# Performance work log

Measured on AMD Instinct MI355X. Metric: run time of the kernel, lower is better.

Reference implementation:

```python
import jax, jax.numpy as jnp
import numpy as np

N = 10000
E = 160000
F_IN = 2000
HEADS = 10
C1 = 128      # layer-1 per-head out channels
C2 = 128      # layer-2 per-head out channels (latent_dim)
NEG_SLOPE = 0.2
EPS = 1e-16


def gat_conv(x, W, att_src, att_dst, bias, src, dst, heads, out_ch, concat):
    """PyG-style GATConv (eval mode, self-loops already included in src/dst).
    x: [N, F_in]; W: [F_in, heads*out_ch]; att_*: [heads, out_ch]; bias: [out_dim].
    src/dst: [E'] edge endpoints (message flows src -> dst).
    """
    n = x.shape[0]
    h = (x @ W).reshape(n, heads, out_ch)              # [N, H, C]
    a_src = jnp.einsum('nhc,hc->nh', h, att_src)       # [N, H]
    a_dst = jnp.einsum('nhc,hc->nh', h, att_dst)       # [N, H]
    e = a_src[src] + a_dst[dst]                        # [E', H]
    e = jax.nn.leaky_relu(e, NEG_SLOPE)
    # segment softmax over incoming edges of each destination node
    m = jax.ops.segment_max(e, dst, num_segments=n)    # [N, H]
    ex = jnp.exp(e - m[dst])
    s = jax.ops.segment_sum(ex, dst, num_segments=n)   # [N, H]
    alpha = ex / (s[dst] + EPS)                        # [E', H]
    msg = h[src] * alpha[:, :, None]                   # [E', H, C]
    out = jax.ops.segment_sum(msg, dst, num_segments=n)  # [N, H, C]
    out = out.reshape(n, heads * out_ch) if concat else out.mean(axis=1)
    return out + bias


def setup_inputs() -> dict:
    key = jax.random.key(0)
    ks = jax.random.split(key, 10)
    glorot = lambda k, shape: jax.random.normal(k, shape, jnp.float32) * np.sqrt(2.0 / (shape[0] + shape[-1]))
    x = jax.random.normal(ks[0], (N, F_IN), jnp.float32)
    edge_index = jax.random.randint(ks[1], (2, E), 0, N, jnp.int64)
    W1 = glorot(ks[2], (F_IN, HEADS * C1))
    att_src1 = glorot(ks[3], (HEADS, C1))
    att_dst1 = glorot(ks[4], (HEADS, C1))
    b1 = jnp.zeros((HEADS * C1,), jnp.float32)
    W2 = glorot(ks[5], (HEADS * C1, HEADS * C2))
    att_src2 = glorot(ks[6], (HEADS, C2))
    att_dst2 = glorot(ks[7], (HEADS, C2))
    b2 = jnp.zeros((C2,), jnp.float32)
    return dict(x=x, edge_index=edge_index, W1=W1, att_src1=att_src1,
                att_dst1=att_dst1, b1=b1, W2=W2, att_src2=att_src2,
                att_dst2=att_dst2, b2=b2)


def reference(x, edge_index, W1, att_src1, att_dst1, b1, W2, att_src2, att_dst2, b2):
    n = x.shape[0]
    loops = jnp.arange(n, dtype=edge_index.dtype)
    src = jnp.concatenate([edge_index[0], loops])  # add self-loops (PyG default)
    dst = jnp.concatenate([edge_index[1], loops])
    h = jax.nn.relu(gat_conv(x, W1, att_src1, att_dst1, b1, src, dst, HEADS, C1, True))
    z = jax.nn.relu(gat_conv(h, W2, att_src2, att_dst2, b2, src, dst, HEADS, C2, False))
    return z
```

## Files before the change

kernel.cpp:

```cpp
#include <hip/hip_runtime.h>

typedef unsigned short u16;
typedef __attribute__((ext_vector_type(8))) short bf16x8;
typedef __attribute__((ext_vector_type(4))) float f32x4;
typedef __attribute__((ext_vector_type(4))) unsigned u32x4;

#define NN    10000
#define EE    160000
#define ET    170000
#define FIN   2000
#define MPAD  10112
#define K1PAD 2048
#define NH    1280
#define HEADS 10
#define NT    10
#define NWG   790

__device__ __forceinline__ u16 f32_to_bf16(float f) {
    unsigned u = __float_as_uint(f);
    unsigned r = (u + 0x7fffu + ((u >> 16) & 1u)) >> 16;
    return (u16)r;
}
__device__ __forceinline__ float bf16lo(unsigned pv) { return __uint_as_float(pv << 16); }
__device__ __forceinline__ float bf16hi(unsigned pv) { return __uint_as_float(pv & 0xffff0000u); }

__device__ __forceinline__ void gload16(const u16* g, u16* l) {
    __builtin_amdgcn_global_load_lds(
        (const __attribute__((address_space(1))) void*)g,
        (__attribute__((address_space(3))) void*)l, 16, 0, 0);
}

__global__ __launch_bounds__(256) void k_prep(const float* __restrict__ x,
                                              uint2* __restrict__ A1,
                                              const float* __restrict__ W1,
                                              u16* __restrict__ B1t) {
    __shared__ float tile[32][33];
    const int bid = blockIdx.x;
    const int t = threadIdx.x;
    if (bid < 2048) {
        const int total = MPAD * (K1PAD / 4);
        for (int idx = bid * 256 + t; idx < total; idx += 2048 * 256) {
            int r = idx >> 9;
            int c = (idx & 511) << 2;
            float4 v = make_float4(0.f, 0.f, 0.f, 0.f);
            if (r < NN && c < FIN) v = *(const float4*)(x + (size_t)r * FIN + c);
            uint2 p;
            p.x = (unsigned)f32_to_bf16(v.x) | ((unsigned)f32_to_bf16(v.y) << 16);
            p.y = (unsigned)f32_to_bf16(v.z) | ((unsigned)f32_to_bf16(v.w) << 16);
            A1[idx] = p;
        }
        return;
    }
    const int tx = t & 31, ty = t >> 5;
    int b = bid - 2048;
    int k0 = (b & 63) * 32, n0 = (b >> 6) * 32;
    #pragma unroll
    for (int i = 0; i < 32; i += 8) {
        int k = k0 + ty + i;
        tile[ty + i][tx] = (k < FIN) ? W1[(size_t)k * NH + n0 + tx] : 0.f;
    }
    __syncthreads();
    #pragma unroll
    for (int i = 0; i < 32; i += 8) {
        int n = n0 + ty + i, k = k0 + tx;
        B1t[(size_t)n * K1PAD + k] = f32_to_bf16(tile[tx][ty + i]);
    }
}

__global__ __launch_bounds__(256) void k_prepW2(const float* __restrict__ W2,
                                                u16* __restrict__ B2t) {
    __shared__ float tile[32][33];
    const int t = threadIdx.x;
    const int tx = t & 31, ty = t >> 5;
    int b = blockIdx.x;
    int k0 = (b % 40) * 32, n0 = (b / 40) * 32;
    #pragma unroll
    for (int i = 0; i < 32; i += 8)
        tile[ty + i][tx] = W2[(size_t)(k0 + ty + i) * NH + n0 + tx];
    __syncthreads();
    #pragma unroll
    for (int i = 0; i < 32; i += 8) {
        int n = n0 + ty + i, k = k0 + tx;
        B2t[(size_t)n * NH + k] = f32_to_bf16(tile[tx][ty + i]);
    }
}

__global__ __launch_bounds__(512) void k_gemm(const u16* __restrict__ A,
                                              const u16* __restrict__ Bt,
                                              u16* __restrict__ Chm,
                                              const int Kpad, const int kTiles) {
    __shared__ __attribute__((aligned(16))) u16 S[32768];
    const int bid = blockIdx.x;
    const int xcd = bid & 7, idx = bid >> 3;
    const int q = NWG >> 3, r = NWG & 7;
    const int L = (xcd < r) ? (xcd * (q + 1) + idx)
                            : (r * (q + 1) + (xcd - r) * q + idx);
    const size_t m0 = (size_t)(L / NT) * 128, n0 = (size_t)(L % NT) * 128;

    const int t = threadIdx.x;
    const int lane = t & 63;
    const int wave = t >> 6;
    const int wr = wave >> 2, wc = wave & 3;

    f32x4 acc[4][2] = {};

    const int srow = t >> 3;
    const int klocal = (((t & 7) ^ ((t >> 3) & 7)) << 3);
    const u16* aRow = A + (m0 + srow) * (size_t)Kpad + klocal;
    const u16* bRow = Bt + (n0 + srow) * (size_t)Kpad + klocal;
    const size_t rStep = (size_t)64 * Kpad;

#define STAGE(kt_, bufb_) do {                                                   \
        char* db = (char*)S + (bufb_) + wave * 1024;                             \
        const u16* aP = aRow + (size_t)(kt_) * 64;                               \
        const u16* bP = bRow + (size_t)(kt_) * 64;                               \
        gload16(aP,         (u16*)(db));                                         \
        gload16(aP + rStep, (u16*)(db + 8192));                                  \
        gload16(bP,         (u16*)(db + 16384));                                 \
        gload16(bP + rStep, (u16*)(db + 24576));                                 \
    } while (0)

    STAGE(0, 0);

    const int rl = lane & 15;
    const int kchunk = lane >> 4;
    const int xorv = (rl & 7) << 4;
    const int aBase0 = (wr * 64 + rl) * 128;
    const int bBase0 = (wc * 32 + rl) * 128;
    const char* Sb = (const char*)S;

    for (int kt = 0; kt < kTiles; ++kt) {
        asm volatile("s_waitcnt vmcnt(0)" ::: "memory");
        __builtin_amdgcn_s_barrier();
        if (kt + 1 < kTiles) STAGE(kt + 1, ((kt + 1) & 1) * 32768);
        const int bufo = (kt & 1) * 32768;
        #pragma unroll
        for (int ks = 0; ks < 2; ++ks) {
            const int px = (ks * 64 + kchunk * 16) ^ xorv;
            bf16x8 af[4], bfr[2];
            #pragma unroll
            for (int mf = 0; mf < 4; ++mf)
                af[mf] = *(const bf16x8*)(Sb + bufo + aBase0 + mf * 2048 + px);
            #pragma unroll
            for (int nf = 0; nf < 2; ++nf)
                bfr[nf] = *(const bf16x8*)(Sb + bufo + 16384 + bBase0 + nf * 2048 + px);
            #pragma unroll
            for (int mf = 0; mf < 4; ++mf)
                #pragma unroll
                for (int nf = 0; nf < 2; ++nf)
                    acc[mf][nf] = __builtin_amdgcn_mfma_f32_16x16x32_bf16(
                        af[mf], bfr[nf], acc[mf][nf], 0, 0, 0);
        }
    }
#undef STAGE

    u16* Cb = Chm + (size_t)(n0 >> 7) * (MPAD << 7);
    #pragma unroll
    for (int mf = 0; mf < 4; ++mf)
        #pragma unroll
        for (int i = 0; i < 4; ++i) {
            size_t row = m0 + wr * 64 + mf * 16 + (lane >> 4) * 4 + i;
            u16* crow = Cb + row * 128 + wc * 32 + rl;
            #pragma unroll
            for (int nf = 0; nf < 2; ++nf)
                crow[nf * 16] = f32_to_bf16(acc[mf][nf][i]);
        }
}

__global__ __launch_bounds__(256) void k_attn(const u16* __restrict__ Hhm,
                                              const float* __restrict__ att_s,
                                              const float* __restrict__ att_d,
                                              float* __restrict__ a_src,
                                              float* __restrict__ a_dst) {
    const int lane = threadIdx.x & 63;
    const int n = blockIdx.x * 4 + (threadIdx.x >> 6);
    if (n >= NN) return;
    const unsigned* Hd = (const unsigned*)Hhm;
    #pragma unroll
    for (int h = 0; h < HEADS; ++h) {
        unsigned pv = Hd[((size_t)h * MPAD + n) * 64 + lane];
        float v0 = bf16lo(pv), v1 = bf16hi(pv);
        int c = h * 128 + lane * 2;
        float s = v0 * att_s[c] + v1 * att_s[c + 1];
        float d = v0 * att_d[c] + v1 * att_d[c + 1];
        #pragma unroll
        for (int o = 32; o; o >>= 1) { s += __shfl_xor(s, o); d += __shfl_xor(d, o); }
        if (lane == 0) { a_src[h * NN + n] = s; a_dst[h * NN + n] = d; }
    }
}

__global__ void k_count(const int* __restrict__ ei, int* __restrict__ deg) {
    int e = blockIdx.x * blockDim.x + threadIdx.x;
    if (e >= ET) return;
    int d = (e < EE) ? ei[EE + e] : (e - EE);
    atomicAdd(&deg[d], 1);
}

__global__ __launch_bounds__(1024) void k_scan(const int* __restrict__ deg,
                                               int* __restrict__ off,
                                               int* __restrict__ cursor) {
    __shared__ int wt[16];
    const int t = threadIdx.x, lane = t & 63, w = t >> 6;
    const int lo = t * 10;
    const int hi = (lo + 10 < NN) ? lo + 10 : NN;
    int s = 0;
    for (int i = lo; i < hi; ++i) s += deg[i];
    int x = s;
    #pragma unroll
    for (int o = 1; o < 64; o <<= 1) { int y = __shfl_up(x, o); if (lane >= o) x += y; }
    if (lane == 63) wt[w] = x;
    __syncthreads();
    int wp = 0;
    for (int k = 0; k < w; ++k) wp += wt[k];
    int run = wp + x - s;
    for (int i = lo; i < hi; ++i) { off[i] = run; cursor[i] = run; run += deg[i]; }
    if (t == 1023) off[NN] = wp + x;
}

__global__ void k_scatter(const int* __restrict__ ei, int* __restrict__ cursor,
                          int* __restrict__ csr_src) {
    int e = blockIdx.x * blockDim.x + threadIdx.x;
    if (e >= ET) return;
    int s = (e < EE) ? ei[e] : (e - EE);
    int d = (e < EE) ? ei[EE + e] : (e - EE);
    int pos = atomicAdd(&cursor[d], 1);
    csr_src[pos] = s;
}

template <int LAYER>
__global__ __launch_bounds__(256) void k_agg(const u16* __restrict__ Hhm,
                                             const float* __restrict__ a_src,
                                             const float* __restrict__ a_dst,
                                             const int* __restrict__ off,
                                             const int* __restrict__ csr,
                                             const float* __restrict__ bias,
                                             unsigned* __restrict__ outp) {
    const int bid = blockIdx.x;
    if (LAYER == 1 && bid >= 6256) {
        int idx = (bid - 6256) * 256 + threadIdx.x;
        if (idx < 112 * 640) outp[(size_t)NN * 640 + idx] = 0u;
        return;
    }
    const int xcd = bid & 7, slot = bid >> 3;
    const int wv = threadIdx.x >> 6, lane = threadIdx.x & 63;
    const int u = slot * 4 + wv;
    if (u >= 3125) return;
    int h, qd;
    if (u < 2500) { h = xcd; qd = u; }
    else {
        int qg = xcd * 625 + (u - 2500);
        h = 8 + (qg >= 2500);
        qd = (qg >= 2500) ? qg - 2500 : qg;
    }
    const int g = lane >> 4, l = lane & 15;
    const int n = qd * 4 + g;
    const int beg = off[n], end = off[n + 1];
    const u16* Hh = Hhm + (size_t)h * (MPAD * 128);
    const float* asl = a_src + (size_t)h * NN;
    const float ad = a_dst[(size_t)h * NN + n];

    float acc[8] = {};
    float den = 0.f;
    int i = beg;
    for (; i + 3 < end; i += 4) {
        const int s0 = csr[i], s1 = csr[i + 1], s2 = csr[i + 2], s3 = csr[i + 3];
        const float a0 = asl[s0], a1 = asl[s1], a2 = asl[s2], a3 = asl[s3];
        const u32x4 v0 = *(const u32x4*)(Hh + (size_t)s0 * 128 + l * 8);
        const u32x4 v1 = *(const u32x4*)(Hh + (size_t)s1 * 128 + l * 8);
        const u32x4 v2 = *(const u32x4*)(Hh + (size_t)s2 * 128 + l * 8);
        const u32x4 v3 = *(const u32x4*)(Hh + (size_t)s3 * 128 + l * 8);
        float e0 = a0 + ad; e0 = (e0 >= 0.f) ? e0 : 0.2f * e0;
        float e1 = a1 + ad; e1 = (e1 >= 0.f) ? e1 : 0.2f * e1;
        float e2 = a2 + ad; e2 = (e2 >= 0.f) ? e2 : 0.2f * e2;
        float e3 = a3 + ad; e3 = (e3 >= 0.f) ? e3 : 0.2f * e3;
        const float w0 = __expf(e0), w1 = __expf(e1);
        const float w2 = __expf(e2), w3 = __expf(e3);
        den += (w0 + w1) + (w2 + w3);
        #pragma unroll
        for (int j = 0; j < 4; ++j) {
            acc[2 * j]     = fmaf(bf16lo(v0[j]), w0, acc[2 * j]);
            acc[2 * j + 1] = fmaf(bf16hi(v0[j]), w0, acc[2 * j + 1]);
            acc[2 * j]     = fmaf(bf16lo(v1[j]), w1, acc[2 * j]);
            acc[2 * j + 1] = fmaf(bf16hi(v1[j]), w1, acc[2 * j + 1]);
            acc[2 * j]     = fmaf(bf16lo(v2[j]), w2, acc[2 * j]);
            acc[2 * j + 1] = fmaf(bf16hi(v2[j]), w2, acc[2 * j + 1]);
            acc[2 * j]     = fmaf(bf16lo(v3[j]), w3, acc[2 * j]);
            acc[2 * j + 1] = fmaf(bf16hi(v3[j]), w3, acc[2 * j + 1]);
        }
    }
    for (; i < end; ++i) {
        const int s0 = csr[i];
        float e0 = asl[s0] + ad; e0 = (e0 >= 0.f) ? e0 : 0.2f * e0;
        const float w0 = __expf(e0);
        const u32x4 v0 = *(const u32x4*)(Hh + (size_t)s0 * 128 + l * 8);
        den += w0;
        #pragma unroll
        for (int j = 0; j < 4; ++j) {
            acc[2 * j]     = fmaf(bf16lo(v0[j]), w0, acc[2 * j]);
            acc[2 * j + 1] = fmaf(bf16hi(v0[j]), w0, acc[2 * j + 1]);
        }
    }
    const float si = 1.f / (den + 1e-16f);

    u32x4 pk;
    if (LAYER == 1) {
        const int c = h * 128 + l * 8;
        #pragma unroll
        for (int j = 0; j < 4; ++j) {
            float v0 = fmaxf(fmaf(acc[2 * j],     si, bias[c + 2 * j]),     0.f);
            float v1 = fmaxf(fmaf(acc[2 * j + 1], si, bias[c + 2 * j + 1]), 0.f);
            pk[j] = (unsigned)f32_to_bf16(v0) | ((unsigned)f32_to_bf16(v1) << 16);
        }
        *(u32x4*)(outp + (size_t)n * 640 + h * 64 + l * 4) = pk;
    } else {
        #pragma unroll
        for (int j = 0; j < 4; ++j) {
            pk[j] = (unsigned)f32_to_bf16(acc[2 * j] * si)
                  | ((unsigned)f32_to_bf16(acc[2 * j + 1] * si) << 16);
        }
        *(u32x4*)(outp + (size_t)h * (MPAD * 64) + (size_t)n * 64 + l * 4) = pk;
    }
}

__global__ __launch_bounds__(256) void k_final(const unsigned* __restrict__ Z,
                                               const float* __restrict__ b2,
                                               float* __restrict__ out) {
    int t = blockIdx.x * 256 + threadIdx.x;
    if (t >= NN * 64) return;
    int n = t >> 6, d = t & 63;
    float s0 = 0.f, s1 = 0.f;
    #pragma unroll
    for (int h = 0; h < HEADS; ++h) {
        unsigned pv = Z[(size_t)h * (MPAD * 64) + (size_t)n * 64 + d];
        s0 += bf16lo(pv);
        s1 += bf16hi(pv);
    }
    float2 z;
    z.x = fmaxf(fmaf(s0, 0.1f, b2[2 * d]),     0.f);
    z.y = fmaxf(fmaf(s1, 0.1f, b2[2 * d + 1]), 0.f);
    *(float2*)(out + (size_t)n * 128 + 2 * d) = z;
}

extern "C" void kernel_launch(void* const* d_in, const int* in_sizes, int n_in,
                              void* d_out, int out_size, void* d_ws, size_t ws_size,
                              hipStream_t stream) {
    const float* x   = (const float*)d_in[0];
    const int*   ei  = (const int*)  d_in[1];
    const float* W1  = (const float*)d_in[2];
    const float* as1 = (const float*)d_in[3];
    const float* ad1 = (const float*)d_in[4];
    const float* b1  = (const float*)d_in[5];
    const float* W2  = (const float*)d_in[6];
    const float* as2 = (const float*)d_in[7];
    const float* ad2 = (const float*)d_in[8];
    const float* b2  = (const float*)d_in[9];

    char* ws = (char*)d_ws;
    const size_t A1_OFF  = 0;
    const size_t A2_OFF  = 0;
    const size_t B2T_OFF = (size_t)MPAD * NH * 2;
    const size_t H_OFF   = (size_t)MPAD * K1PAD * 2;
    const size_t B1T_OFF = H_OFF + (size_t)MPAD * NH * 2;
    size_t o = B1T_OFF + (size_t)NH * K1PAD * 2;
    const size_t AS_OFF  = o; o += 400128;
    const size_t AD_OFF  = o; o += 400128;
    const size_t DEG_OFF = o; o += 40064;
    const size_t OFF_OFF = o; o += 40064;
    const size_t CUR_OFF = o; o += 40064;
    const size_t CSR_OFF = o; o += 680064;
    if (ws_size < o) return;

    u16*      A1   = (u16*)(ws + A1_OFF);
    unsigned* A2   = (unsigned*)(ws + A2_OFF);
    u16*      B2t  = (u16*)(ws + B2T_OFF);
    u16*      H    = (u16*)(ws + H_OFF);
    u16*      B1t  = (u16*)(ws + B1T_OFF);
    float*    aS   = (float*)(ws + AS_OFF);
    float*    aD   = (float*)(ws + AD_OFF);
    int*      deg  = (int*)(ws + DEG_OFF);
    int*      offp = (int*)(ws + OFF_OFF);
    int*      cur  = (int*)(ws + CUR_OFF);
    int*      csr  = (int*)(ws + CSR_OFF);

    hipMemsetAsync(deg, 0, NN * sizeof(int), stream);
    k_count<<<(ET + 255) / 256, 256, 0, stream>>>(ei, deg);
    k_scan<<<1, 1024, 0, stream>>>(deg, offp, cur);
    k_scatter<<<(ET + 255) / 256, 256, 0, stream>>>(ei, cur, csr);

    k_prep<<<4608, 256, 0, stream>>>(x, (uint2*)A1, W1, B1t);

    k_gemm<<<NWG, 512, 0, stream>>>(A1, B1t, H, K1PAD, K1PAD / 64);
    k_prepW2<<<1600, 256, 0, stream>>>(W2, B2t);
    k_attn<<<2500, 256, 0, stream>>>(H, as1, ad1, aS, aD);
    k_agg<1><<<6536, 256, 0, stream>>>(H, aS, aD, offp, csr, b1, A2);

    k_gemm<<<NWG, 512, 0, stream>>>((u16*)A2, B2t, H, NH, NH / 64);
    k_attn<<<2500, 256, 0, stream>>>(H, as2, ad2, aS, aD);
    k_agg<2><<<6256, 256, 0, stream>>>(H, aS, aD, offp, csr, b2, A2);
    k_final<<<(NN * 64 + 255) / 256, 256, 0, stream>>>(A2, b2, (float*)d_out);
}
```

Before: 272.2 us.

## Make each GEMM workgroup compute two adjacent N tiles sequentially

Each GEMM workgroup now handles two consecutive 128-column output tiles. It runs one continuous double-buffered K loop over both tiles and writes the first tile's results midway, so the grid halves from 790 to 395 workgroups. This is meant to cut the wave-quantization tail on 256 CUs and keep the pipeline primed across tile boundaries. The cost is fewer concurrent workgroups (395 over 256 CUs is still uneven) and longer serial work per workgroup, with no reuse of A between the two tiles.

```diff
diff --git a/kernel.cpp b/kernel.cpp
--- a/kernel.cpp
+++ b/kernel.cpp
@@ -14,7 +14,7 @@
 #define NH    1280
 #define HEADS 10
 #define NT    10
-#define NWG   790
+#define NWG2  395
 
 __device__ __forceinline__ u16 f32_to_bf16(float f) {
     unsigned u = __float_as_uint(f);
@@ -92,10 +92,12 @@
     __shared__ __attribute__((aligned(16))) u16 S[32768];
     const int bid = blockIdx.x;
     const int xcd = bid & 7, idx = bid >> 3;
-    const int q = NWG >> 3, r = NWG & 7;
-    const int L = (xcd < r) ? (xcd * (q + 1) + idx)
-                            : (r * (q + 1) + (xcd - r) * q + idx);
-    const size_t m0 = (size_t)(L / NT) * 128, n0 = (size_t)(L % NT) * 128;
+    const int q = NWG2 >> 3, rr = NWG2 & 7;
+    const int P = (xcd < rr) ? (xcd * (q + 1) + idx)
+                             : (rr * (q + 1) + (xcd - rr) * q + idx);
+    const int L0 = 2 * P;
+    const size_t m0 = (size_t)(L0 / NT) * 128;
+    const int n0a = (L0 % NT) * 128;
 
     const int t = threadIdx.x;
     const int lane = t & 63;
@@ -107,17 +109,34 @@
     const int srow = t >> 3;
     const int klocal = (((t & 7) ^ ((t >> 3) & 7)) << 3);
     const u16* aRow = A + (m0 + srow) * (size_t)Kpad + klocal;
-    const u16* bRow = Bt + (n0 + srow) * (size_t)Kpad + klocal;
+    const u16* bRow = Bt + (size_t)(n0a + srow) * Kpad + klocal;
     const size_t rStep = (size_t)64 * Kpad;
-
-#define STAGE(kt_, bufb_) do {                                                   \
+    const size_t bTile = (size_t)128 * Kpad;
+
+#define STAGE(j_, bufb_) do {                                                    \
         char* db = (char*)S + (bufb_) + wave * 1024;                             \
-        const u16* aP = aRow + (size_t)(kt_) * 64;                               \
-        const u16* bP = bRow + (size_t)(kt_) * 64;                               \
+        const int jj_ = (j_) < kTiles ? (j_) : (j_) - kTiles;                    \
+        const u16* bR_ = (j_) < kTiles ? bRow : bRow + bTile;                    \
+        const u16* aP = aRow + (size_t)jj_ * 64;                                 \
+        const u16* bP = bR_ + (size_t)jj_ * 64;                                  \
         gload16(aP,         (u16*)(db));                                         \
         gload16(aP + rStep, (u16*)(db + 8192));                                  \
         gload16(bP,         (u16*)(db + 16384));                                 \
         gload16(bP + rStep, (u16*)(db + 24576));                                 \
+    } while (0)
+
+#define EPILOG(ncol_) do {                                                       \
+        u16* Cb_ = Chm + (size_t)((ncol_) >> 7) * (MPAD << 7);                   \
+        _Pragma("unroll")                                                        \
+        for (int mf_ = 0; mf_ < 4; ++mf_)                                        \
+            _Pragma("unroll")                                                    \
+            for (int i_ = 0; i_ < 4; ++i_) {                                     \
+                size_t row_ = m0 + wr * 64 + mf_ * 16 + (lane >> 4) * 4 + i_;    \
+                u16* crow_ = Cb_ + row_ * 128 + wc * 32 + (lane & 15);           \
+                _Pragma("unroll")                                                \
+                for (int nf_ = 0; nf_ < 2; ++nf_)                                \
+                    crow_[nf_ * 16] = f32_to_bf16(acc[mf_][nf_][i_]);            \
+            }                                                                    \
     } while (0)
 
     STAGE(0, 0);
@@ -128,11 +147,12 @@
     const int aBase0 = (wr * 64 + rl) * 128;
     const int bBase0 = (wc * 32 + rl) * 128;
     const char* Sb = (const char*)S;
-
-    for (int kt = 0; kt < kTiles; ++kt) {
+    const int kTotal = 2 * kTiles;
+
+    for (int kt = 0; kt < kTotal; ++kt) {
         asm volatile("s_waitcnt vmcnt(0)" ::: "memory");
         __builtin_amdgcn_s_barrier();
-        if (kt + 1 < kTiles) STAGE(kt + 1, ((kt + 1) & 1) * 32768);
+        if (kt + 1 < kTotal) STAGE(kt + 1, ((kt + 1) & 1) * 32768);
         const int bufo = (kt & 1) * 32768;
         #pragma unroll
         for (int ks = 0; ks < 2; ++ks) {
@@ -151,20 +171,18 @@
                     acc[mf][nf] = __builtin_amdgcn_mfma_f32_16x16x32_bf16(
                         af[mf], bfr[nf], acc[mf][nf], 0, 0, 0);
         }
-    }
+        if (kt == kTiles - 1) {
+            EPILOG(n0a);
+            #pragma unroll
+            for (int mf = 0; mf < 4; ++mf)
+                #pragma unroll
+                for (int nf = 0; nf < 2; ++nf)
+                    acc[mf][nf] = (f32x4){0.f, 0.f, 0.f, 0.f};
+        }
+    }
+    EPILOG(n0a + 128);
 #undef STAGE
-
-    u16* Cb = Chm + (size_t)(n0 >> 7) * (MPAD << 7);
-    #pragma unroll
-    for (int mf = 0; mf < 4; ++mf)
-        #pragma unroll
-        for (int i = 0; i < 4; ++i) {
-            size_t row = m0 + wr * 64 + mf * 16 + (lane >> 4) * 4 + i;
-            u16* crow = Cb + row * 128 + wc * 32 + rl;
-            #pragma unroll
-            for (int nf = 0; nf < 2; ++nf)
-                crow[nf * 16] = f32_to_bf16(acc[mf][nf][i]);
-        }
+#undef EPILOG
 }
 
 __global__ __launch_bounds__(256) void k_attn(const u16* __restrict__ Hhm,
@@ -389,12 +407,12 @@
 
     k_prep<<<4608, 256, 0, stream>>>(x, (uint2*)A1, W1, B1t);
 
-    k_gemm<<<NWG, 512, 0, stream>>>(A1, B1t, H, K1PAD, K1PAD / 64);
+    k_gemm<<<NWG2, 512, 0, stream>>>(A1, B1t, H, K1PAD, K1PAD / 64);
     k_prepW2<<<1600, 256, 0, stream>>>(W2, B2t);
     k_attn<<<2500, 256, 0, stream>>>(H, as1, ad1, aS, aD);
     k_agg<1><<<6536, 256, 0, stream>>>(H, aS, aD, offp, csr, b1, A2);
 
-    k_gemm<<<NWG, 512, 0, stream>>>((u16*)A2, B2t, H, NH, NH / 64);
+    k_gemm<<<NWG2, 512, 0, stream>>>((u16*)A2, B2t, H, NH, NH / 64);
     k_attn<<<2500, 256, 0, stream>>>(H, as2, ad2, aS, aD);
     k_agg<2><<<6256, 256, 0, stream>>>(H, aS, aD, offp, csr, b2, A2);
     k_final<<<(NN * 64 + 255) / 256, 256, 0, stream>>>(A2, b2, (float*)d_out);
```

New measurement: 268.2 us (median of 3 runs). No clear change (-1.5%).
